# Optimization experiments

Hardware: AMD Instinct MI355X
Metric: run time of the kernel (lower is better)

## Reference

```python
import jax, jax.numpy as jnp
import numpy as np

N_EMBD = 512
BLOCK = 512
HEADS = 16
HEAD_DIM = N_EMBD // HEADS
EPS = 1e-5


def _layernorm(x, g, b):
    mu = jnp.mean(x, axis=-1, keepdims=True)
    var = jnp.mean(jnp.square(x - mu), axis=-1, keepdims=True)
    return (x - mu) * jax.lax.rsqrt(var + EPS) * g + b


def setup_inputs() -> dict:
    key = jax.random.key(0)
    ks = jax.random.split(key, 12)
    B, T, C, H, D = 64, BLOCK, N_EMBD, HEADS, HEAD_DIM
    s = lambda fan_in: 1.0 / np.sqrt(fan_in)
    return {
        "x": jax.random.normal(ks[0], (B, T, C), dtype=jnp.float32),
        # per-head projections, stored (H, C, D) so y = einsum('btc,hcd->bhtd')
        "Wq": jax.random.normal(ks[1], (H, C, D), dtype=jnp.float32) * s(C),
        "Wk": jax.random.normal(ks[2], (H, C, D), dtype=jnp.float32) * s(C),
        "Wv": jax.random.normal(ks[3], (H, C, D), dtype=jnp.float32) * s(C),
        "Wp": jax.random.normal(ks[4], (C, C), dtype=jnp.float32) * s(C),
        "bp": jnp.zeros((C,), dtype=jnp.float32),
        "W1": jax.random.normal(ks[5], (C, 4 * C), dtype=jnp.float32) * s(C),
        "b1": jnp.zeros((4 * C,), dtype=jnp.float32),
        "W2": jax.random.normal(ks[6], (4 * C, C), dtype=jnp.float32) * s(4 * C),
        "b2": jnp.zeros((C,), dtype=jnp.float32),
        "g_ln1": jnp.ones((C,), dtype=jnp.float32),
        "b_ln1": jnp.zeros((C,), dtype=jnp.float32),
        "g_ln2": jnp.ones((C,), dtype=jnp.float32),
        "b_ln2": jnp.zeros((C,), dtype=jnp.float32),
    }


def reference(x, Wq, Wk, Wv, Wp, bp, W1, b1, W2, b2, g_ln1, b_ln1, g_ln2, b_ln2):
    B, T, C = x.shape
    h = _layernorm(x, g_ln1, b_ln1)
    q = jnp.einsum('btc,hcd->bhtd', h, Wq)
    k = jnp.einsum('btc,hcd->bhtd', h, Wk)
    v = jnp.einsum('btc,hcd->bhtd', h, Wv)
    wei = jnp.einsum('bhtd,bhsd->bhts', q, k) * (HEAD_DIM ** -0.5)
    causal = jnp.tril(jnp.ones((T, T), dtype=bool))
    wei = jnp.where(causal, wei, -jnp.inf)
    wei = jax.nn.softmax(wei, axis=-1)  # dropout = identity (eval mode)
    out = jnp.einsum('bhts,bhsd->bhtd', wei, v)
    out = out.transpose(0, 2, 1, 3).reshape(B, T, C)  # concat heads
    sa = out @ Wp + bp
    x = x + sa
    h2 = _layernorm(x, g_ln2, b_ln2)
    ff = jax.nn.relu(h2 @ W1 + b1) @ W2 + b2
    return x + ff
```

## Files before the change

### kernel.cpp

```cpp
#include <hip/hip_runtime.h>
#include <stdint.h>


typedef __attribute__((ext_vector_type(8))) short bf16x8;
typedef __attribute__((ext_vector_type(4))) short bf16x4;
typedef __attribute__((ext_vector_type(4))) float f32x4;

__device__ __forceinline__ unsigned short f2bf(float x) {
  union { float f; unsigned u; } v; v.f = x;
  unsigned r = v.u + 0x7fff + ((v.u >> 16) & 1);
  return (unsigned short)(r >> 16);
}

#if __has_builtin(__builtin_amdgcn_exp2f)
__device__ __forceinline__ float exp2fast(float x) { return __builtin_amdgcn_exp2f(x); }
#else
__device__ __forceinline__ float exp2fast(float x) { return exp2f(x); }
#endif

__device__ __forceinline__ unsigned cvtpk(float lo, float hi) {
  unsigned r; asm("v_cvt_pk_bf16_f32 %0, %1, %2" : "=v"(r) : "v"(lo), "v"(hi)); return r;
}

__device__ __forceinline__ f32x4 MFMA32(bf16x8 a, bf16x8 b, f32x4 c) {
  return __builtin_amdgcn_mfma_f32_16x16x32_bf16(a, b, c, 0, 0, 0);
}

#if __has_builtin(__builtin_amdgcn_mfma_f32_16x16x16bf16_1k)
__device__ __forceinline__ f32x4 MFMA16(bf16x4 a, bf16x4 b, f32x4 c) {
  return __builtin_amdgcn_mfma_f32_16x16x16bf16_1k(a, b, c, 0, 0, 0);
}
#else
__device__ __forceinline__ f32x4 MFMA16(bf16x4 a, bf16x4 b, f32x4 c) {
  f32x4 d;
  asm volatile("v_mfma_f32_16x16x16_bf16 %0, %1, %2, %3\n\ts_nop 7\n\ts_nop 3"
               : "=v"(d) : "v"(a), "v"(b), "v"(c));
  return d;
}
#endif

__device__ __forceinline__ void gload_lds16(const void* g, void* l) {
  __builtin_amdgcn_global_load_lds(
      (const __attribute__((address_space(1))) unsigned int*)(uintptr_t)g,
      (__attribute__((address_space(3))) unsigned int*)(unsigned)(uintptr_t)l,
      16, 0, 0);
}

#define WAITV8() do { asm volatile("s_waitcnt vmcnt(8)" ::: "memory"); } while (0)
#define WAITV0() do { asm volatile("s_waitcnt vmcnt(0)" ::: "memory"); } while (0)
#define WAITL0() do { asm volatile("s_waitcnt lgkmcnt(0)" ::: "memory"); } while (0)
#define SBAR()   __builtin_amdgcn_s_barrier()
#define SCHED0() __builtin_amdgcn_sched_barrier(0)

__global__ __launch_bounds__(256) void prep_qkv_w(
    const float* __restrict__ Wq, const float* __restrict__ Wk,
    const float* __restrict__ Wv, unsigned short* __restrict__ dst)
{
  __shared__ float tile[64 * 33];
  const int b = blockIdx.x;
  const int q = b / 128, hh = (b >> 3) & 15, kt = (b & 7) << 6;
  const float* W = (q == 0) ? Wq : ((q == 1) ? Wk : Wv);
  const int t = threadIdx.x;
  const int rr = t >> 2, ch = (t & 3) << 3;
  const float* sp = W + ((size_t)hh * 512 + kt + rr) * 32 + ch;
  float4 v0 = *(const float4*)(sp), v1 = *(const float4*)(sp + 4);
  float* dp = &tile[rr * 33 + ch];
  dp[0] = v0.x; dp[1] = v0.y; dp[2] = v0.z; dp[3] = v0.w;
  dp[4] = v1.x; dp[5] = v1.y; dp[6] = v1.z; dp[7] = v1.w;
  __syncthreads();
  const int d = t >> 3, toct = (t & 7) << 3;
  bf16x8 o;
#pragma unroll
  for (int j = 0; j < 8; ++j) o[j] = (short)f2bf(tile[(toct + j) * 33 + d]);
  *(bf16x8*)(dst + ((size_t)q * 512 + hh * 32 + d) * 512 + kt + toct) = o;
}

__global__ __launch_bounds__(256) void transpose_cast(
    const float* __restrict__ src, unsigned short* __restrict__ dst, int Kd, int Nd)
{
  __shared__ float tile[64 * 65];
  const int nk = Kd >> 6;
  const int kt = (blockIdx.x % nk) << 6, nt = (blockIdx.x / nk) << 6;
  const int t = threadIdx.x;
  const int rr = t >> 2, ch = (t & 3) << 4;
  const float* sp = src + (size_t)(kt + rr) * Nd + nt + ch;
  float* dp = &tile[rr * 65 + ch];
#pragma unroll
  for (int c = 0; c < 4; ++c) {
    float4 v = *(const float4*)(sp + c * 4);
    dp[c * 4 + 0] = v.x; dp[c * 4 + 1] = v.y; dp[c * 4 + 2] = v.z; dp[c * 4 + 3] = v.w;
  }
  __syncthreads();
  const int nn = t >> 2, c2 = (t & 3) << 4;
  bf16x8 o0, o1;
#pragma unroll
  for (int j = 0; j < 8; ++j) {
    o0[j] = (short)f2bf(tile[(c2 + j) * 65 + nn]);
    o1[j] = (short)f2bf(tile[(c2 + 8 + j) * 65 + nn]);
  }
  unsigned short* op = dst + (size_t)(nt + nn) * Kd + kt + c2;
  *(bf16x8*)(op) = o0;
  *(bf16x8*)(op + 8) = o1;
}

__global__ __launch_bounds__(256) void ln_kernel(
    const float* __restrict__ x, const float* __restrict__ g,
    const float* __restrict__ b, unsigned short* __restrict__ out)
{
  const int lane = threadIdx.x & 63;
  const size_t row = (size_t)blockIdx.x * 4 + (threadIdx.x >> 6);
  const float* xp = x + row * 512 + lane * 8;
  float xv[8] __attribute__((aligned(16)));
  *(float4*)(xv)     = *(const float4*)(xp);
  *(float4*)(xv + 4) = *(const float4*)(xp + 4);
  float s = 0.f, s2 = 0.f;
#pragma unroll
  for (int j = 0; j < 8; ++j) { s += xv[j]; s2 += xv[j] * xv[j]; }
#pragma unroll
  for (int m = 1; m < 64; m <<= 1) { s += __shfl_xor(s, m); s2 += __shfl_xor(s2, m); }
  float mean = s * (1.f / 512.f);
  float rstd = rsqrtf(fmaxf(s2 * (1.f / 512.f) - mean * mean, 0.f) + 1e-5f);
  float gv[8] __attribute__((aligned(16))), bv[8] __attribute__((aligned(16)));
  *(float4*)(gv)     = *(const float4*)(g + lane * 8);
  *(float4*)(gv + 4) = *(const float4*)(g + lane * 8 + 4);
  *(float4*)(bv)     = *(const float4*)(b + lane * 8);
  *(float4*)(bv + 4) = *(const float4*)(b + lane * 8 + 4);
  bf16x8 o;
#pragma unroll
  for (int j = 0; j < 8; ++j) o[j] = (short)f2bf((xv[j] - mean) * rstd * gv[j] + bv[j]);
  *(bf16x8*)(out + row * 512 + lane * 8) = o;
}

__global__ __launch_bounds__(256) void vt_kernel(
    const unsigned short* __restrict__ vnat, unsigned short* __restrict__ vt)
{
  __shared__ unsigned short tile[64 * 36];
  const int bh = blockIdx.x >> 3, tt = (blockIdx.x & 7) << 6;
  const int tid = threadIdx.x;
  const int rr = tid >> 2, ch = tid & 3;
  bf16x8 v = *(const bf16x8*)(vnat + ((size_t)bh * 512 + tt + rr) * 32 + ch * 8);
  unsigned short* dst = &tile[rr * 36 + ch * 8];
#pragma unroll
  for (int j = 0; j < 8; ++j) dst[j] = (unsigned short)v[j];
  __syncthreads();
  const int d = tid >> 3, toct = (tid & 7) << 3;
  union { unsigned short s[8]; bf16x8 v8; } o;
#pragma unroll
  for (int j = 0; j < 8; ++j) o.s[j] = tile[(toct + j) * 36 + d];
  *(bf16x8*)(vt + ((size_t)bh * 32 + d) * 512 + tt + toct) = o.v8;
}

template <int MODE>
__device__ __forceinline__ void gemm256_body(
    const unsigned short* __restrict__ A, const unsigned short* __restrict__ Bt,
    int N, int K, int nby,
    unsigned short* __restrict__ obf, float* __restrict__ of32,
    const float* __restrict__ bias, const float* __restrict__ resid,
    unsigned short* __restrict__ vout)
{
  __shared__ __align__(16) unsigned short As[2][256 * 64];
  __shared__ __align__(16) unsigned short Bs[2][256 * 64];
  const int tid = threadIdx.x, lane = tid & 63, wid = tid >> 6;
  const int wr = wid >> 2, wc = wid & 3;
  const int r = lane & 15, hq = lane >> 4;

  const int qq = gridDim.x >> 3;
  const int swz = (blockIdx.x & 7) * qq + (blockIdx.x >> 3);
  const int bx = swz / nby, by = swz - bx * nby;
  const int brow = bx * 256, bcol = by * 256;
  const int nkt = K >> 6;

  const int srow = wid * 32 + (lane >> 3);
  const int schunk = ((lane & 7) ^ ((lane >> 3) & 7)) * 8;
  const unsigned short* Asrc = A + (size_t)(brow + srow) * K + schunk;
  const unsigned short* Bsrc = Bt + (size_t)(bcol + srow) * K + schunk;

  auto STAGE_A = [&](int t, int buf) {
    const unsigned short* as_ = Asrc + t * 64;
    char* al_ = (char*)(&As[buf][0]) + wid * 4096;
#pragma unroll
    for (int g = 0; g < 4; ++g) gload_lds16(as_ + (size_t)g * 8 * K, al_ + g * 1024);
  };
  auto STAGE_B = [&](int t, int buf) {
    const unsigned short* bs_ = Bsrc + t * 64;
    char* bl_ = (char*)(&Bs[buf][0]) + wid * 4096;
#pragma unroll
    for (int g = 0; g < 4; ++g) gload_lds16(bs_ + (size_t)g * 8 * K, bl_ + g * 1024);
  };

  const int x0 = ((hq) ^ (r & 7)) * 16;
  const int x1 = ((4 + hq) ^ (r & 7)) * 16;
  const int abase = (wr * 128 + r) * 128;
  const int bbase = (wc * 64 + r) * 128;

  f32x4 acc[8][4] = {};
  bf16x8 af[4][2], bfa[2][2], bfb[2][2];

  STAGE_A(0, 0); STAGE_B(0, 0);
  STAGE_A(1, 1); STAGE_B(1, 1);
  WAITV8(); SCHED0();
  SBAR();

  for (int t = 0; t < nkt; ++t) {
    const char* Ab = (const char*)(&As[t & 1][0]);
    const char* Bb = (const char*)(&Bs[t & 1][0]);
#pragma unroll
    for (int m = 0; m < 4; ++m) {
      af[m][0] = *(const bf16x8*)(Ab + abase + m * 2048 + x0);
      af[m][1] = *(const bf16x8*)(Ab + abase + m * 2048 + x1);
    }
#pragma unroll
    for (int n = 0; n < 2; ++n) {
      bfa[n][0] = *(const bf16x8*)(Bb + bbase + n * 2048 + x0);
      bfa[n][1] = *(const bf16x8*)(Bb + bbase + n * 2048 + x1);
    }
    WAITL0(); SCHED0();
    __builtin_amdgcn_s_setprio(1);
#pragma unroll
    for (int m = 0; m < 4; ++m)
#pragma unroll
      for (int n = 0; n < 2; ++n) {
        acc[m][n] = MFMA32(af[m][0], bfa[n][0], acc[m][n]);
        acc[m][n] = MFMA32(af[m][1], bfa[n][1], acc[m][n]);
      }
    __builtin_amdgcn_s_setprio(0);
    SBAR();
#pragma unroll
    for (int n = 0; n < 2; ++n) {
      bfb[n][0] = *(const bf16x8*)(Bb + bbase + (n + 2) * 2048 + x0);
      bfb[n][1] = *(const bf16x8*)(Bb + bbase + (n + 2) * 2048 + x1);
    }
    WAITL0(); SCHED0();
    __builtin_amdgcn_s_setprio(1);
#pragma unroll
    for (int m = 0; m < 4; ++m)
#pragma unroll
      for (int n = 0; n < 2; ++n) {
        acc[m][n + 2] = MFMA32(af[m][0], bfb[n][0], acc[m][n + 2]);
        acc[m][n + 2] = MFMA32(af[m][1], bfb[n][1], acc[m][n + 2]);
      }
    __builtin_amdgcn_s_setprio(0);
    SBAR();
#pragma unroll
    for (int m = 0; m < 4; ++m) {
      af[m][0] = *(const bf16x8*)(Ab + abase + 8192 + m * 2048 + x0);
      af[m][1] = *(const bf16x8*)(Ab + abase + 8192 + m * 2048 + x1);
    }
    if (t + 2 < nkt) STAGE_B(t + 2, t & 1);
    WAITL0(); SCHED0();
    __builtin_amdgcn_s_setprio(1);
#pragma unroll
    for (int m = 0; m < 4; ++m)
#pragma unroll
      for (int n = 0; n < 2; ++n) {
        acc[4 + m][n] = MFMA32(af[m][0], bfa[n][0], acc[4 + m][n]);
        acc[4 + m][n] = MFMA32(af[m][1], bfa[n][1], acc[4 + m][n]);
      }
    __builtin_amdgcn_s_setprio(0);
    SBAR();
    if (t + 2 < nkt) STAGE_A(t + 2, t & 1);
    __builtin_amdgcn_s_setprio(1);
#pragma unroll
    for (int m = 0; m < 4; ++m)
#pragma unroll
      for (int n = 0; n < 2; ++n) {
        acc[4 + m][n + 2] = MFMA32(af[m][0], bfb[n][0], acc[4 + m][n + 2]);
        acc[4 + m][n + 2] = MFMA32(af[m][1], bfb[n][1], acc[4 + m][n + 2]);
      }
    __builtin_amdgcn_s_setprio(0);
    if (t + 2 < nkt) { WAITV8(); } else { WAITV0(); }
    SCHED0();
    SBAR();
  }

#pragma unroll
  for (int m = 0; m < 8; ++m)
#pragma unroll
    for (int n = 0; n < 4; ++n) {
      const int row0 = brow + wr * 128 + m * 16 + hq * 4;
      const int col = bcol + wc * 64 + n * 16 + r;
#pragma unroll
      for (int q2 = 0; q2 < 4; ++q2) {
        const int row = row0 + q2;
        float v = acc[m][n][q2];
        if (MODE == 1) {
          const int which = col >> 9, hh = (col >> 5) & 15, dd = col & 31;
          const int bb = row >> 9, tt = row & 511;
          const size_t off = ((((size_t)bb) * 16 + hh) * 512 + tt) * 32 + dd;
          if (which < 2) {
            if (which == 0) v *= 0.25503521f;
            obf[(size_t)which * 16777216 + off] = f2bf(v);
          } else
            vout[off] = f2bf(v);
        } else if (MODE == 2) {
          v += bias[col] + resid[(size_t)row * N + col];
          of32[(size_t)row * N + col] = v;
        } else if (MODE == 3) {
          v = fmaxf(v + bias[col], 0.f);
          obf[(size_t)row * N + col] = f2bf(v);
        }
      }
    }
}

__global__ __launch_bounds__(512, 2) void qkv_gemm(
    const unsigned short* __restrict__ A, const unsigned short* __restrict__ Bt,
    int N, int K, int nby, unsigned short* __restrict__ obf,
    unsigned short* __restrict__ vout)
{ gemm256_body<1>(A, Bt, N, K, nby, obf, nullptr, nullptr, nullptr, vout); }

__global__ __launch_bounds__(512, 2) void proj_gemm(
    const unsigned short* __restrict__ A, const unsigned short* __restrict__ Bt,
    int N, int K, int nby, float* __restrict__ of32,
    const float* __restrict__ bias, const float* __restrict__ resid)
{ gemm256_body<2>(A, Bt, N, K, nby, nullptr, of32, bias, resid, nullptr); }

__global__ __launch_bounds__(512, 2) void ffn1_gemm(
    const unsigned short* __restrict__ A, const unsigned short* __restrict__ Bt,
    int N, int K, int nby, unsigned short* __restrict__ obf,
    const float* __restrict__ bias)
{ gemm256_body<3>(A, Bt, N, K, nby, obf, nullptr, bias, nullptr, nullptr); }

__global__ __launch_bounds__(512, 2) void ffn2_gemm(
    const unsigned short* __restrict__ A, const unsigned short* __restrict__ Bt,
    int N, int K, int nby, float* __restrict__ of32,
    const float* __restrict__ bias, const float* __restrict__ resid)
{ gemm256_body<2>(A, Bt, N, K, nby, nullptr, of32, bias, resid, nullptr); }

__global__ __launch_bounds__(512, 4) void attn_kernel(
    const unsigned short* __restrict__ Qb, const unsigned short* __restrict__ Kb,
    const unsigned short* __restrict__ Vt, unsigned short* __restrict__ att)
{
  __shared__ __align__(16) unsigned short Ks[512 * 32];
  __shared__ __align__(16) unsigned short Vs[32 * 512];
  const int tid = threadIdx.x, lane = tid & 63, wid = tid >> 6;
  const int bh = blockIdx.x;
  const int r = lane & 15, hq = lane >> 4;
  const unsigned short* Kg = Kb + (size_t)bh * (512 * 32);
  const unsigned short* Vg = Vt + (size_t)bh * (32 * 512);
#pragma unroll
  for (int it = 0; it < 4; ++it) {
    const int c = it * 512 + tid;
    gload_lds16(Kg + c * 8, (char*)Ks + (it * 512 + wid * 64) * 16);
    const int d = c >> 6, sb = c & 63;
    gload_lds16(Vg + d * 512 + (sb ^ (d & 15)) * 8, (char*)Vs + (it * 512 + wid * 64) * 16);
  }
  __syncthreads();

  const f32x4 z = {0.f, 0.f, 0.f, 0.f};
  for (int p = 0; p < 4; ++p) {
    const int t0 = (((p >> 1) << 4) + ((p & 1) ? 15 - wid : wid)) << 4;
    const bf16x8 qf = *(const bf16x8*)(Qb + ((size_t)bh * 512 + t0 + r) * 32 + hq * 8);
    f32x4 o0 = z, o1 = z;
    float m = -1e30f, l = 0.f;
    const int s0m = t0 & ~31;
    for (int s0 = 0; s0 <= s0m; s0 += 32) {
      f32x4 st0 = MFMA32(*(const bf16x8*)((const char*)Ks + (s0 + r) * 64 + hq * 16), qf, z);
      f32x4 st1 = MFMA32(*(const bf16x8*)((const char*)Ks + (s0 + 16 + r) * 64 + hq * 16), qf, z);
      if (s0 == s0m) {
        const int qq = t0 + r;
#pragma unroll
        for (int j = 0; j < 4; ++j) {
          if (s0 + 4 * hq + j > qq)      st0[j] = -1e30f;
          if (s0 + 16 + 4 * hq + j > qq) st1[j] = -1e30f;
        }
      }
      float mx = fmaxf(fmaxf(fmaxf(st0[0], st0[1]), fmaxf(st0[2], st0[3])),
                       fmaxf(fmaxf(st1[0], st1[1]), fmaxf(st1[2], st1[3])));
      mx = fmaxf(mx, __shfl_xor(mx, 16));
      mx = fmaxf(mx, __shfl_xor(mx, 32));
      if (!__all(mx <= m + 8.f)) {
        const float mn = fmaxf(m, mx);
        const float f = exp2fast(m - mn);
        m = mn; l *= f; o0 *= f; o1 *= f;
      }
      float p0[4], p1[4];
#pragma unroll
      for (int j = 0; j < 4; ++j) {
        p0[j] = exp2fast(st0[j] - m);
        p1[j] = exp2fast(st1[j] - m);
      }
      float rs = ((p0[0] + p0[1]) + (p0[2] + p0[3])) + ((p1[0] + p1[1]) + (p1[2] + p1[3]));
      rs += __shfl_xor(rs, 16);
      rs += __shfl_xor(rs, 32);
      l += rs;
      union { unsigned u[2]; bf16x4 v; } a0, a1;
      a0.u[0] = cvtpk(p0[0], p0[1]); a0.u[1] = cvtpk(p0[2], p0[3]);
      a1.u[0] = cvtpk(p1[0], p1[1]); a1.u[1] = cvtpk(p1[2], p1[3]);
      const int lb = (s0 >> 3) + (hq >> 1);
      const char* vb = (const char*)Vs + (hq & 1) * 8;
      o0 = MFMA16(a0.v, *(const bf16x4*)(vb + r * 1024 + ((lb) ^ r) * 16), o0);
      o0 = MFMA16(a1.v, *(const bf16x4*)(vb + r * 1024 + ((lb + 2) ^ r) * 16), o0);
      o1 = MFMA16(a0.v, *(const bf16x4*)(vb + (r + 16) * 1024 + ((lb) ^ r) * 16), o1);
      o1 = MFMA16(a1.v, *(const bf16x4*)(vb + (r + 16) * 1024 + ((lb + 2) ^ r) * 16), o1);
    }
    const size_t ob = ((size_t)(bh >> 4) * 512) * 512 + (size_t)((bh & 15) * 32);
#pragma unroll
    for (int j = 0; j < 4; ++j) {
      const float li = 1.f / __shfl(l, 4 * hq + j);
      const size_t rowb = ob + (size_t)(t0 + 4 * hq + j) * 512;
      att[rowb + r]      = f2bf(o0[j] * li);
      att[rowb + 16 + r] = f2bf(o1[j] * li);
    }
  }
}

extern "C" void kernel_launch(void* const* d_in, const int* in_sizes, int n_in,
                              void* d_out, int out_size, void* d_ws, size_t ws_size,
                              hipStream_t stream)
{
  const float* x   = (const float*)d_in[0];
  const float* Wq  = (const float*)d_in[1];
  const float* Wk  = (const float*)d_in[2];
  const float* Wv  = (const float*)d_in[3];
  const float* Wp  = (const float*)d_in[4];
  const float* bp  = (const float*)d_in[5];
  const float* W1  = (const float*)d_in[6];
  const float* b1  = (const float*)d_in[7];
  const float* W2  = (const float*)d_in[8];
  const float* b2  = (const float*)d_in[9];
  const float* g1  = (const float*)d_in[10];
  const float* bb1 = (const float*)d_in[11];
  const float* g2  = (const float*)d_in[12];
  const float* bb2 = (const float*)d_in[13];
  float* out = (float*)d_out;

  char* ws = (char*)d_ws;
  unsigned short* h    = (unsigned short*)(ws);
  unsigned short* wqkv = (unsigned short*)(ws + 33554432);
  unsigned short* wp   = (unsigned short*)(ws + 35127296);
  unsigned short* w1   = (unsigned short*)(ws + 35651584);
  unsigned short* w2   = (unsigned short*)(ws + 37748736);
  unsigned short* qk   = (unsigned short*)(ws + 39845888);
  unsigned short* vt   = qk + (size_t)2 * 16777216;
  unsigned short* att  = vt + 16777216;
  unsigned short* vnat = att;
  unsigned short* mid  = qk;
  if (ws_size < 174063616) return;

  prep_qkv_w<<<384, 256, 0, stream>>>(Wq, Wk, Wv, wqkv);
  transpose_cast<<<64, 256, 0, stream>>>(Wp, wp, 512, 512);
  transpose_cast<<<256, 256, 0, stream>>>(W1, w1, 512, 2048);
  transpose_cast<<<256, 256, 0, stream>>>(W2, w2, 2048, 512);

  ln_kernel<<<8192, 256, 0, stream>>>(x, g1, bb1, h);

  qkv_gemm<<<768, 512, 0, stream>>>(h, wqkv, 1536, 512, 6, qk, vnat);

  vt_kernel<<<8192, 256, 0, stream>>>(vnat, vt);

  attn_kernel<<<1024, 512, 0, stream>>>(qk, qk + 16777216, vt, att);

  proj_gemm<<<256, 512, 0, stream>>>(att, wp, 512, 512, 2, out, bp, x);

  ln_kernel<<<8192, 256, 0, stream>>>(out, g2, bb2, h);

  ffn1_gemm<<<1024, 512, 0, stream>>>(h, w1, 2048, 512, 8, mid, b1);

  ffn2_gemm<<<256, 512, 0, stream>>>(mid, w2, 512, 2048, 2, out, b2, out);
}
```

Before: 390.8 us.

## Make GEMMs persistent over multiple tiles with cross-tile prefetch pipeline

Converts the 256x256 GEMM kernel into a persistent form where each of 256 blocks processes P consecutive output tiles, using a flattened tile-by-k index so the double-buffered LDS prefetch continues across tile boundaries. The QKV and FFN1 grids shrink to 256 blocks (one wave on 256 CUs), removing tail/launch-wave effects and overlapping the next tile's loads with the current epilogue. K and tile counts become compile-time constants. It adds an accumulator reset and epilogue inside the loop, which raises register pressure, and tile assignment by contiguous ranges may change L2 reuse.

```diff
diff --git a/kernel.cpp b/kernel.cpp
--- a/kernel.cpp
+++ b/kernel.cpp
@@ -150,42 +150,43 @@
   *(bf16x8*)(vt + ((size_t)bh * 32 + d) * 512 + tt + toct) = o.v8;
 }
 
-template <int MODE>
-__device__ __forceinline__ void gemm256_body(
+template <int MODE, int P, int KT, int NBY>
+__device__ __forceinline__ void gemm_persist(
     const unsigned short* __restrict__ A, const unsigned short* __restrict__ Bt,
-    int N, int K, int nby,
+    int N,
     unsigned short* __restrict__ obf, float* __restrict__ of32,
     const float* __restrict__ bias, const float* __restrict__ resid,
     unsigned short* __restrict__ vout)
 {
+  constexpr int K = KT * 64;
+  constexpr int TOT = P * KT;
   __shared__ __align__(16) unsigned short As[2][256 * 64];
   __shared__ __align__(16) unsigned short Bs[2][256 * 64];
   const int tid = threadIdx.x, lane = tid & 63, wid = tid >> 6;
   const int wr = wid >> 2, wc = wid & 3;
   const int r = lane & 15, hq = lane >> 4;
 
-  const int qq = gridDim.x >> 3;
-  const int swz = (blockIdx.x & 7) * qq + (blockIdx.x >> 3);
-  const int bx = swz / nby, by = swz - bx * nby;
-  const int brow = bx * 256, bcol = by * 256;
-  const int nkt = K >> 6;
+  const int tau0 = (blockIdx.x & 7) * (32 * P) + (blockIdx.x >> 3) * P;
 
   const int srow = wid * 32 + (lane >> 3);
   const int schunk = ((lane & 7) ^ ((lane >> 3) & 7)) * 8;
-  const unsigned short* Asrc = A + (size_t)(brow + srow) * K + schunk;
-  const unsigned short* Bsrc = Bt + (size_t)(bcol + srow) * K + schunk;
-
-  auto STAGE_A = [&](int t, int buf) {
-    const unsigned short* as_ = Asrc + t * 64;
-    char* al_ = (char*)(&As[buf][0]) + wid * 4096;
-#pragma unroll
-    for (int g = 0; g < 4; ++g) gload_lds16(as_ + (size_t)g * 8 * K, al_ + g * 1024);
+
+  auto STAGE_A = [&](int g2) {
+    const int m2 = g2 / KT, kt2 = g2 % KT;
+    const int bx = (tau0 + m2) / NBY;
+    const unsigned short* src = A + (size_t)(bx * 256 + srow) * K + kt2 * 64 + schunk;
+    char* dst = (char*)(&As[g2 & 1][0]) + wid * 4096;
+#pragma unroll
+    for (int g = 0; g < 4; ++g) gload_lds16(src + (size_t)g * 8 * K, dst + g * 1024);
   };
-  auto STAGE_B = [&](int t, int buf) {
-    const unsigned short* bs_ = Bsrc + t * 64;
-    char* bl_ = (char*)(&Bs[buf][0]) + wid * 4096;
-#pragma unroll
-    for (int g = 0; g < 4; ++g) gload_lds16(bs_ + (size_t)g * 8 * K, bl_ + g * 1024);
+  auto STAGE_B = [&](int g2) {
+    const int m2 = g2 / KT, kt2 = g2 % KT;
+    const int tau = tau0 + m2;
+    const int by = tau - (tau / NBY) * NBY;
+    const unsigned short* src = Bt + (size_t)(by * 256 + srow) * K + kt2 * 64 + schunk;
+    char* dst = (char*)(&Bs[g2 & 1][0]) + wid * 4096;
+#pragma unroll
+    for (int g = 0; g < 4; ++g) gload_lds16(src + (size_t)g * 8 * K, dst + g * 1024);
   };
 
   const int x0 = ((hq) ^ (r & 7)) * 16;
@@ -196,136 +197,146 @@
   f32x4 acc[8][4] = {};
   bf16x8 af[4][2], bfa[2][2], bfb[2][2];
 
-  STAGE_A(0, 0); STAGE_B(0, 0);
-  STAGE_A(1, 1); STAGE_B(1, 1);
+  STAGE_A(0); STAGE_B(0);
+  STAGE_A(1); STAGE_B(1);
   WAITV8(); SCHED0();
   SBAR();
 
-  for (int t = 0; t < nkt; ++t) {
-    const char* Ab = (const char*)(&As[t & 1][0]);
-    const char* Bb = (const char*)(&Bs[t & 1][0]);
-#pragma unroll
-    for (int m = 0; m < 4; ++m) {
-      af[m][0] = *(const bf16x8*)(Ab + abase + m * 2048 + x0);
-      af[m][1] = *(const bf16x8*)(Ab + abase + m * 2048 + x1);
+#pragma unroll 1
+  for (int p = 0; p < P; ++p) {
+#pragma unroll 2
+    for (int t = 0; t < KT; ++t) {
+      const int g = p * KT + t;
+      const int g2 = g + 2;
+      const char* Ab = (const char*)(&As[g & 1][0]);
+      const char* Bb = (const char*)(&Bs[g & 1][0]);
+#pragma unroll
+      for (int m = 0; m < 4; ++m) {
+        af[m][0] = *(const bf16x8*)(Ab + abase + m * 2048 + x0);
+        af[m][1] = *(const bf16x8*)(Ab + abase + m * 2048 + x1);
+      }
+#pragma unroll
+      for (int n = 0; n < 2; ++n) {
+        bfa[n][0] = *(const bf16x8*)(Bb + bbase + n * 2048 + x0);
+        bfa[n][1] = *(const bf16x8*)(Bb + bbase + n * 2048 + x1);
+      }
+      WAITL0(); SCHED0();
+      __builtin_amdgcn_s_setprio(1);
+#pragma unroll
+      for (int m = 0; m < 4; ++m)
+#pragma unroll
+        for (int n = 0; n < 2; ++n) {
+          acc[m][n] = MFMA32(af[m][0], bfa[n][0], acc[m][n]);
+          acc[m][n] = MFMA32(af[m][1], bfa[n][1], acc[m][n]);
+        }
+      __builtin_amdgcn_s_setprio(0);
+      SBAR();
+#pragma unroll
+      for (int n = 0; n < 2; ++n) {
+        bfb[n][0] = *(const bf16x8*)(Bb + bbase + (n + 2) * 2048 + x0);
+        bfb[n][1] = *(const bf16x8*)(Bb + bbase + (n + 2) * 2048 + x1);
+      }
+      WAITL0(); SCHED0();
+      __builtin_amdgcn_s_setprio(1);
+#pragma unroll
+      for (int m = 0; m < 4; ++m)
+#pragma unroll
+        for (int n = 0; n < 2; ++n) {
+          acc[m][n + 2] = MFMA32(af[m][0], bfb[n][0], acc[m][n + 2]);
+          acc[m][n + 2] = MFMA32(af[m][1], bfb[n][1], acc[m][n + 2]);
+        }
+      __builtin_amdgcn_s_setprio(0);
+      SBAR();
+#pragma unroll
+      for (int m = 0; m < 4; ++m) {
+        af[m][0] = *(const bf16x8*)(Ab + abase + 8192 + m * 2048 + x0);
+        af[m][1] = *(const bf16x8*)(Ab + abase + 8192 + m * 2048 + x1);
+      }
+      if (g2 < TOT) STAGE_B(g2);
+      WAITL0(); SCHED0();
+      __builtin_amdgcn_s_setprio(1);
+#pragma unroll
+      for (int m = 0; m < 4; ++m)
+#pragma unroll
+        for (int n = 0; n < 2; ++n) {
+          acc[4 + m][n] = MFMA32(af[m][0], bfa[n][0], acc[4 + m][n]);
+          acc[4 + m][n] = MFMA32(af[m][1], bfa[n][1], acc[4 + m][n]);
+        }
+      __builtin_amdgcn_s_setprio(0);
+      SBAR();
+      if (g2 < TOT) STAGE_A(g2);
+      __builtin_amdgcn_s_setprio(1);
+#pragma unroll
+      for (int m = 0; m < 4; ++m)
+#pragma unroll
+        for (int n = 0; n < 2; ++n) {
+          acc[4 + m][n + 2] = MFMA32(af[m][0], bfb[n][0], acc[4 + m][n + 2]);
+          acc[4 + m][n + 2] = MFMA32(af[m][1], bfb[n][1], acc[4 + m][n + 2]);
+        }
+      __builtin_amdgcn_s_setprio(0);
+      if (g2 < TOT) { WAITV8(); } else { WAITV0(); }
+      SCHED0();
+      SBAR();
     }
-#pragma unroll
-    for (int n = 0; n < 2; ++n) {
-      bfa[n][0] = *(const bf16x8*)(Bb + bbase + n * 2048 + x0);
-      bfa[n][1] = *(const bf16x8*)(Bb + bbase + n * 2048 + x1);
+
+    {
+      const int tau = tau0 + p;
+      const int bx = tau / NBY, by = tau - bx * NBY;
+      const int brow = bx << 8, bcol = by << 8;
+#pragma unroll
+      for (int m = 0; m < 8; ++m)
+#pragma unroll
+        for (int n = 0; n < 4; ++n) {
+          const int row0 = brow + wr * 128 + m * 16 + hq * 4;
+          const int col = bcol + wc * 64 + n * 16 + r;
+#pragma unroll
+          for (int q2 = 0; q2 < 4; ++q2) {
+            const int row = row0 + q2;
+            float v = acc[m][n][q2];
+            if (MODE == 1) {
+              const int which = col >> 9, hh = (col >> 5) & 15, dd = col & 31;
+              const int bb = row >> 9, tt = row & 511;
+              const size_t off = ((((size_t)bb) * 16 + hh) * 512 + tt) * 32 + dd;
+              if (which < 2) {
+                if (which == 0) v *= 0.25503521f;
+                obf[(size_t)which * 16777216 + off] = f2bf(v);
+              } else
+                vout[off] = f2bf(v);
+            } else if (MODE == 2) {
+              v += bias[col] + resid[(size_t)row * N + col];
+              of32[(size_t)row * N + col] = v;
+            } else if (MODE == 3) {
+              v = fmaxf(v + bias[col], 0.f);
+              obf[(size_t)row * N + col] = f2bf(v);
+            }
+            acc[m][n][q2] = 0.f;
+          }
+        }
     }
-    WAITL0(); SCHED0();
-    __builtin_amdgcn_s_setprio(1);
-#pragma unroll
-    for (int m = 0; m < 4; ++m)
-#pragma unroll
-      for (int n = 0; n < 2; ++n) {
-        acc[m][n] = MFMA32(af[m][0], bfa[n][0], acc[m][n]);
-        acc[m][n] = MFMA32(af[m][1], bfa[n][1], acc[m][n]);
-      }
-    __builtin_amdgcn_s_setprio(0);
-    SBAR();
-#pragma unroll
-    for (int n = 0; n < 2; ++n) {
-      bfb[n][0] = *(const bf16x8*)(Bb + bbase + (n + 2) * 2048 + x0);
-      bfb[n][1] = *(const bf16x8*)(Bb + bbase + (n + 2) * 2048 + x1);
-    }
-    WAITL0(); SCHED0();
-    __builtin_amdgcn_s_setprio(1);
-#pragma unroll
-    for (int m = 0; m < 4; ++m)
-#pragma unroll
-      for (int n = 0; n < 2; ++n) {
-        acc[m][n + 2] = MFMA32(af[m][0], bfb[n][0], acc[m][n + 2]);
-        acc[m][n + 2] = MFMA32(af[m][1], bfb[n][1], acc[m][n + 2]);
-      }
-    __builtin_amdgcn_s_setprio(0);
-    SBAR();
-#pragma unroll
-    for (int m = 0; m < 4; ++m) {
-      af[m][0] = *(const bf16x8*)(Ab + abase + 8192 + m * 2048 + x0);
-      af[m][1] = *(const bf16x8*)(Ab + abase + 8192 + m * 2048 + x1);
-    }
-    if (t + 2 < nkt) STAGE_B(t + 2, t & 1);
-    WAITL0(); SCHED0();
-    __builtin_amdgcn_s_setprio(1);
-#pragma unroll
-    for (int m = 0; m < 4; ++m)
-#pragma unroll
-      for (int n = 0; n < 2; ++n) {
-        acc[4 + m][n] = MFMA32(af[m][0], bfa[n][0], acc[4 + m][n]);
-        acc[4 + m][n] = MFMA32(af[m][1], bfa[n][1], acc[4 + m][n]);
-      }
-    __builtin_amdgcn_s_setprio(0);
-    SBAR();
-    if (t + 2 < nkt) STAGE_A(t + 2, t & 1);
-    __builtin_amdgcn_s_setprio(1);
-#pragma unroll
-    for (int m = 0; m < 4; ++m)
-#pragma unroll
-      for (int n = 0; n < 2; ++n) {
-        acc[4 + m][n + 2] = MFMA32(af[m][0], bfb[n][0], acc[4 + m][n + 2]);
-        acc[4 + m][n + 2] = MFMA32(af[m][1], bfb[n][1], acc[4 + m][n + 2]);
-      }
-    __builtin_amdgcn_s_setprio(0);
-    if (t + 2 < nkt) { WAITV8(); } else { WAITV0(); }
-    SCHED0();
-    SBAR();
   }
-
-#pragma unroll
-  for (int m = 0; m < 8; ++m)
-#pragma unroll
-    for (int n = 0; n < 4; ++n) {
-      const int row0 = brow + wr * 128 + m * 16 + hq * 4;
-      const int col = bcol + wc * 64 + n * 16 + r;
-#pragma unroll
-      for (int q2 = 0; q2 < 4; ++q2) {
-        const int row = row0 + q2;
-        float v = acc[m][n][q2];
-        if (MODE == 1) {
-          const int which = col >> 9, hh = (col >> 5) & 15, dd = col & 31;
-          const int bb = row >> 9, tt = row & 511;
-          const size_t off = ((((size_t)bb) * 16 + hh) * 512 + tt) * 32 + dd;
-          if (which < 2) {
-            if (which == 0) v *= 0.25503521f;
-            obf[(size_t)which * 16777216 + off] = f2bf(v);
-          } else
-            vout[off] = f2bf(v);
-        } else if (MODE == 2) {
-          v += bias[col] + resid[(size_t)row * N + col];
-          of32[(size_t)row * N + col] = v;
-        } else if (MODE == 3) {
-          v = fmaxf(v + bias[col], 0.f);
-          obf[(size_t)row * N + col] = f2bf(v);
-        }
-      }
-    }
 }
 
 __global__ __launch_bounds__(512, 2) void qkv_gemm(
     const unsigned short* __restrict__ A, const unsigned short* __restrict__ Bt,
-    int N, int K, int nby, unsigned short* __restrict__ obf,
-    unsigned short* __restrict__ vout)
-{ gemm256_body<1>(A, Bt, N, K, nby, obf, nullptr, nullptr, nullptr, vout); }
+    unsigned short* __restrict__ obf, unsigned short* __restrict__ vout)
+{ gemm_persist<1, 3, 8, 6>(A, Bt, 1536, obf, nullptr, nullptr, nullptr, vout); }
 
 __global__ __launch_bounds__(512, 2) void proj_gemm(
     const unsigned short* __restrict__ A, const unsigned short* __restrict__ Bt,
-    int N, int K, int nby, float* __restrict__ of32,
-    const float* __restrict__ bias, const float* __restrict__ resid)
-{ gemm256_body<2>(A, Bt, N, K, nby, nullptr, of32, bias, resid, nullptr); }
+    float* __restrict__ of32, const float* __restrict__ bias,
+    const float* __restrict__ resid)
+{ gemm_persist<2, 1, 8, 2>(A, Bt, 512, nullptr, of32, bias, resid, nullptr); }
 
 __global__ __launch_bounds__(512, 2) void ffn1_gemm(
     const unsigned short* __restrict__ A, const unsigned short* __restrict__ Bt,
-    int N, int K, int nby, unsigned short* __restrict__ obf,
-    const float* __restrict__ bias)
-{ gemm256_body<3>(A, Bt, N, K, nby, obf, nullptr, bias, nullptr, nullptr); }
+    unsigned short* __restrict__ obf, const float* __restrict__ bias)
+{ gemm_persist<3, 4, 8, 8>(A, Bt, 2048, obf, nullptr, bias, nullptr, nullptr); }
 
 __global__ __launch_bounds__(512, 2) void ffn2_gemm(
     const unsigned short* __restrict__ A, const unsigned short* __restrict__ Bt,
-    int N, int K, int nby, float* __restrict__ of32,
-    const float* __restrict__ bias, const float* __restrict__ resid)
-{ gemm256_body<2>(A, Bt, N, K, nby, nullptr, of32, bias, resid, nullptr); }
+    float* __restrict__ of32, const float* __restrict__ bias,
+    const float* __restrict__ resid)
+{ gemm_persist<2, 1, 32, 2>(A, Bt, 512, nullptr, of32, bias, resid, nullptr); }
 
 __global__ __launch_bounds__(512, 4) void attn_kernel(
     const unsigned short* __restrict__ Qb, const unsigned short* __restrict__ Kb,
@@ -445,17 +456,17 @@
 
   ln_kernel<<<8192, 256, 0, stream>>>(x, g1, bb1, h);
 
-  qkv_gemm<<<768, 512, 0, stream>>>(h, wqkv, 1536, 512, 6, qk, vnat);
+  qkv_gemm<<<256, 512, 0, stream>>>(h, wqkv, qk, vnat);
 
   vt_kernel<<<8192, 256, 0, stream>>>(vnat, vt);
 
   attn_kernel<<<1024, 512, 0, stream>>>(qk, qk + 16777216, vt, att);
 
-  proj_gemm<<<256, 512, 0, stream>>>(att, wp, 512, 512, 2, out, bp, x);
+  proj_gemm<<<256, 512, 0, stream>>>(att, wp, out, bp, x);
 
   ln_kernel<<<8192, 256, 0, stream>>>(out, g2, bb2, h);
 
-  ffn1_gemm<<<1024, 512, 0, stream>>>(h, w1, 2048, 512, 8, mid, b1);
-
-  ffn2_gemm<<<256, 512, 0, stream>>>(mid, w2, 512, 2048, 2, out, b2, out);
-}
+  ffn1_gemm<<<256, 512, 0, stream>>>(h, w1, mid, b1);
+
+  ffn2_gemm<<<256, 512, 0, stream>>>(mid, w2, out, b2, out);
+}
```

Result: no change. 387.3 us (-0.9%).
